# Optimization experiments

Hardware: AMD Instinct MI355X
Metric: run time of the kernel (lower is better)

## Reference

```python
import jax, jax.numpy as jnp
import numpy as np
import math

DIM = 1024
HEADS = 16
HEAD_DIM = DIM // HEADS
SCALE = math.sqrt(HEAD_DIM)


def setup_inputs() -> dict:
    key = jax.random.key(0)
    ks = jax.random.split(key, 7)
    B, T, C = 2, 2048, DIM
    w = 0.02
    return {
        "x": jax.random.normal(ks[0], (B, T, C), dtype=jnp.float32),
        "W_Q": jax.random.normal(ks[1], (C, C), dtype=jnp.float32) * w,
        "W_K": jax.random.normal(ks[2], (C, C), dtype=jnp.float32) * w,
        "W_V": jax.random.normal(ks[3], (C, C), dtype=jnp.float32) * w,
        "W_K_prime": jax.random.normal(ks[4], (C, C), dtype=jnp.float32) * w,
        "W_O": jax.random.normal(ks[5], (C, C), dtype=jnp.float32) * w,
        "alpha": jnp.float32(0.5),
    }


def _heads(y, B, T):
    # (B,T,C) -> (B,H,T,D)
    return y.reshape(B, T, HEADS, HEAD_DIM).transpose(0, 2, 1, 3)


def reference(x, W_Q, W_K, W_V, W_K_prime, W_O, alpha):
    B, T, C = x.shape
    # nn.Linear(no bias): y = x @ W.T
    q = _heads(x @ W_Q.T, B, T)
    k = _heads(x @ W_K.T, B, T)
    v = _heads(x @ W_V.T, B, T)
    kp = _heads(x @ W_K_prime.T, B, T)

    # Standard branch
    scores = jnp.einsum("bhqd,bhkd->bhqk", q, k) / SCALE
    attn = jax.nn.softmax(scores, axis=-1)  # dropout = identity (eval mode)
    out_std = jnp.einsum("bhqk,bhkd->bhqd", attn, v)

    # K' branch
    scores_p = jnp.einsum("bhqd,bhkd->bhqk", q, kp) / SCALE
    attn_p = jax.nn.softmax(scores_p, axis=-1)
    out_p = jnp.einsum("bhqk,bhkd->bhqd", attn_p, v)

    out = alpha * out_std + (1.0 - alpha) * out_p
    out = out.transpose(0, 2, 1, 3).reshape(B, T, C)
    return out @ W_O.T
```

## Files before the change

kernel.cpp:

```cpp
#include <hip/hip_runtime.h>
#include <math.h>

#define TSZ 2048
#define CDIM 1024

typedef __attribute__((ext_vector_type(8))) short s16x8;
typedef __attribute__((ext_vector_type(4))) float f32x4;
typedef __attribute__((ext_vector_type(16))) float f32x16;
typedef __attribute__((ext_vector_type(2))) unsigned int u32x2;
typedef __attribute__((ext_vector_type(4))) unsigned int u32x4;

#define QSCL 0.1803368801f

__device__ __forceinline__ short f2bf(float f) {
    union { float f; unsigned u; } v; v.f = f;
    unsigned r = v.u + 0x7fffu + ((v.u >> 16) & 1u);
    return (short)(r >> 16);
}
__device__ __forceinline__ unsigned cvtpk(float lo, float hi) {
    unsigned r;
    asm("v_cvt_pk_bf16_f32 %0, %1, %2" : "=v"(r) : "v"(lo), "v"(hi));
    return r;
}
__device__ __forceinline__ float fexp2(float x) {
    float r;
    asm("v_exp_f32 %0, %1" : "=v"(r) : "v"(x));
    return r;
}
__device__ __forceinline__ s16x8 u2s(u32x4 u) {
    union { u32x4 u; s16x8 s; } c; c.u = u; return c.s;
}
__device__ __forceinline__ f32x16 mfma32(s16x8 a, s16x8 b, f32x16 c) {
    return __builtin_amdgcn_mfma_f32_32x32x16_bf16(a, b, c, 0, 0, 0);
}

__global__ void cast_f32_bf16(const float* __restrict__ src, short* __restrict__ dst, int n4) {
    int i = blockIdx.x * blockDim.x + threadIdx.x;
    int stride = gridDim.x * blockDim.x;
    for (; i < n4; i += stride) {
        float4 v = reinterpret_cast<const float4*>(src)[i];
        short4 o;
        o.x = f2bf(v.x); o.y = f2bf(v.y); o.z = f2bf(v.z); o.w = f2bf(v.w);
        reinterpret_cast<short4*>(dst)[i] = o;
    }
}

__global__ void cast_w5(const float* __restrict__ w0, const float* __restrict__ w1,
                        const float* __restrict__ w2, const float* __restrict__ w3,
                        const float* __restrict__ w4,
                        short* __restrict__ o0, short* __restrict__ o1,
                        short* __restrict__ o2, short* __restrict__ o3,
                        short* __restrict__ o4) {
    int z = blockIdx.y;
    const float* s = z == 0 ? w0 : z == 1 ? w1 : z == 2 ? w2 : z == 3 ? w3 : w4;
    short* d = z == 0 ? o0 : z == 1 ? o1 : z == 2 ? o2 : z == 3 ? o3 : o4;
    int i = blockIdx.x * blockDim.x + threadIdx.x;
    float4 v = reinterpret_cast<const float4*>(s)[i];
    short4 o;
    o.x = f2bf(v.x); o.y = f2bf(v.y); o.z = f2bf(v.z); o.w = f2bf(v.w);
    reinterpret_cast<short4*>(d)[i] = o;
}

__device__ __forceinline__ void gload16(const short* g, short* l) {
    __builtin_amdgcn_global_load_lds((const __attribute__((address_space(1))) void*)g,
                                     (__attribute__((address_space(3))) void*)l, 16, 0, 0);
}

__device__ __forceinline__ void stage128x64(short* lds_t, const short* g, int ld, int tid, int w) {
    #pragma unroll
    for (int call = 0; call < 4; ++call) {
        int c = call * 256 + tid;
        int row = c >> 3;
        int sc = (c & 7) ^ (row & 7);
        gload16(g + (size_t)row * ld + sc * 8, lds_t + (size_t)(call * 256 + w * 64) * 8);
    }
}

__device__ __forceinline__ void stage64x64(short* lds_t, const short* g, int ld, int tid, int w) {
    #pragma unroll
    for (int call = 0; call < 2; ++call) {
        int c = call * 256 + tid;
        int row = c >> 3;
        int sc = (c & 7) ^ (row & 7);
        gload16(g + (size_t)row * ld + sc * 8, lds_t + (size_t)(call * 256 + w * 64) * 8);
    }
}

__device__ __forceinline__ s16x8 frag_read(const short* tile, int row, int kc) {
    const char* p = (const char*)tile + row * 128 + (((kc ^ (row & 7)) & 7) << 4);
    return *reinterpret_cast<const s16x8*>(p);
}

__global__ __launch_bounds__(256) void gemm4_proj(
    const short* __restrict__ xb,
    const short* __restrict__ w0, const short* __restrict__ w1,
    const short* __restrict__ w2, const short* __restrict__ w3,
    short* __restrict__ o0, short* __restrict__ o1,
    short* __restrict__ o2, short* __restrict__ o3)
{
    __shared__ short sA[128 * 64], sB[128 * 64];
    int tid = threadIdx.x, lane = tid & 63, w = tid >> 6;
    int wrow = w >> 1, wcol = w & 1;
    int z = blockIdx.y;
    const short* W = z == 0 ? w0 : z == 1 ? w1 : z == 2 ? w2 : w3;
    short* outp = z == 0 ? o0 : z == 1 ? o1 : z == 2 ? o2 : o3;
    int bx = blockIdx.x;
    bx = (bx & 7) * 32 + (bx >> 3);
    int r0 = (bx >> 3) * 128;
    int c0 = (bx & 7) * 128;

    f32x4 zero = {0.f, 0.f, 0.f, 0.f};
    f32x4 acc[4][4];
    #pragma unroll
    for (int i = 0; i < 4; ++i)
        #pragma unroll
        for (int j = 0; j < 4; ++j) acc[i][j] = zero;

    for (int kt = 0; kt < 16; ++kt) {
        __syncthreads();
        stage128x64(sA, xb + (size_t)r0 * CDIM + kt * 64, CDIM, tid, w);
        stage128x64(sB, W + (size_t)c0 * CDIM + kt * 64, CDIM, tid, w);
        __syncthreads();
        #pragma unroll
        for (int ks = 0; ks < 2; ++ks) {
            int kc = ks * 4 + (lane >> 4);
            s16x8 af[4], bfr[4];
            #pragma unroll
            for (int mt = 0; mt < 4; ++mt) af[mt] = frag_read(sA, wrow * 64 + mt * 16 + (lane & 15), kc);
            #pragma unroll
            for (int nt = 0; nt < 4; ++nt) bfr[nt] = frag_read(sB, wcol * 64 + nt * 16 + (lane & 15), kc);
            #pragma unroll
            for (int mt = 0; mt < 4; ++mt)
                #pragma unroll
                for (int nt = 0; nt < 4; ++nt)
                    acc[mt][nt] = __builtin_amdgcn_mfma_f32_16x16x32_bf16(af[mt], bfr[nt], acc[mt][nt], 0, 0, 0);
        }
    }

    bool vt_mode = (z == 2);
    float oscale = (z == 0) ? QSCL : 1.0f;
    #pragma unroll
    for (int mt = 0; mt < 4; ++mt)
        #pragma unroll
        for (int nt = 0; nt < 4; ++nt)
            #pragma unroll
            for (int jr = 0; jr < 4; ++jr) {
                int gi = r0 + wrow * 64 + mt * 16 + ((lane >> 4) << 2) + jr;
                int gn = c0 + wcol * 64 + nt * 16 + (lane & 15);
                short v = f2bf(acc[mt][nt][jr] * oscale);
                int b = gi >> 11, t = gi & 2047, h = gn >> 6, d = gn & 63;
                size_t off;
                if (!vt_mode) off = ((size_t)(b * 16 + h) * TSZ + t) * 64 + d;
                else          off = ((size_t)(b * 16 + h) * 64 + d) * TSZ + t;
                outp[off] = v;
            }
}

__global__ __launch_bounds__(256) void gemm_final(
    const short* __restrict__ ab, const short* __restrict__ wo, float* __restrict__ out)
{
    __shared__ short sA[128 * 64], sB[128 * 64];
    int tid = threadIdx.x, lane = tid & 63, w = tid >> 6;
    int wrow = w >> 1, wcol = w & 1;
    int bx = blockIdx.x;
    bx = (bx & 7) * 32 + (bx >> 3);
    int r0 = (bx >> 3) * 128;
    int c0 = (bx & 7) * 128;

    f32x4 zero = {0.f, 0.f, 0.f, 0.f};
    f32x4 acc[4][4];
    #pragma unroll
    for (int i = 0; i < 4; ++i)
        #pragma unroll
        for (int j = 0; j < 4; ++j) acc[i][j] = zero;

    for (int kt = 0; kt < 16; ++kt) {
        __syncthreads();
        stage128x64(sA, ab + (size_t)r0 * CDIM + kt * 64, CDIM, tid, w);
        stage128x64(sB, wo + (size_t)c0 * CDIM + kt * 64, CDIM, tid, w);
        __syncthreads();
        #pragma unroll
        for (int ks = 0; ks < 2; ++ks) {
            int kc = ks * 4 + (lane >> 4);
            s16x8 af[4], bfr[4];
            #pragma unroll
            for (int mt = 0; mt < 4; ++mt) af[mt] = frag_read(sA, wrow * 64 + mt * 16 + (lane & 15), kc);
            #pragma unroll
            for (int nt = 0; nt < 4; ++nt) bfr[nt] = frag_read(sB, wcol * 64 + nt * 16 + (lane & 15), kc);
            #pragma unroll
            for (int mt = 0; mt < 4; ++mt)
                #pragma unroll
                for (int nt = 0; nt < 4; ++nt)
                    acc[mt][nt] = __builtin_amdgcn_mfma_f32_16x16x32_bf16(af[mt], bfr[nt], acc[mt][nt], 0, 0, 0);
        }
    }

    #pragma unroll
    for (int mt = 0; mt < 4; ++mt)
        #pragma unroll
        for (int nt = 0; nt < 4; ++nt)
            #pragma unroll
            for (int jr = 0; jr < 4; ++jr) {
                int gi = r0 + wrow * 64 + mt * 16 + ((lane >> 4) << 2) + jr;
                int gn = c0 + wcol * 64 + nt * 16 + (lane & 15);
                out[(size_t)gi * CDIM + gn] = acc[mt][nt][jr];
            }
}

__global__ __launch_bounds__(256, 2) void attn_fused(
    const short* __restrict__ q, const short* __restrict__ k, const short* __restrict__ kp,
    const short* __restrict__ vt, const float* __restrict__ alphap, short* __restrict__ aout)
{
    __shared__ short sK[2][64 * 64], sKp[2][64 * 64], sV[2][64 * 64];
    int tid = threadIdx.x, lane = tid & 63, w = tid >> 6;
    int h = lane >> 5, l31 = lane & 31;

    int id = blockIdx.x + gridDim.x * blockIdx.y;
    int nid = (id & 7) * 64 + (id >> 3);
    int bh = nid >> 4;
    int qt0 = (nid & 15) * 128;

    const short* Q  = q  + (size_t)bh * TSZ * 64;
    const short* K  = k  + (size_t)bh * TSZ * 64;
    const short* Kp = kp + (size_t)bh * TSZ * 64;
    const short* Vt = vt + (size_t)bh * 64 * TSZ;

    int qrow = qt0 + w * 32 + l31;
    s16x8 qf[4];
    #pragma unroll
    for (int s = 0; s < 4; ++s)
        qf[s] = *reinterpret_cast<const s16x8*>(Q + (size_t)qrow * 64 + s * 16 + h * 8);

    f32x16 o[2][2];
    #pragma unroll
    for (int br = 0; br < 2; ++br)
        #pragma unroll
        for (int dt = 0; dt < 2; ++dt)
            #pragma unroll
            for (int r = 0; r < 16; ++r) o[br][dt][r] = 0.f;
    float lloc[2] = {0.f, 0.f};

    stage64x64(sK[0],  K, 64, tid, w);
    stage64x64(sKp[0], Kp, 64, tid, w);
    stage64x64(sV[0],  Vt, TSZ, tid, w);
    __syncthreads();

    int cur = 0;
    for (int kt = 0; kt < 32; ++kt) {
        if (kt < 31) {
            int t0n = (kt + 1) * 64;
            stage64x64(sK[cur ^ 1],  K  + (size_t)t0n * 64, 64, tid, w);
            stage64x64(sKp[cur ^ 1], Kp + (size_t)t0n * 64, 64, tid, w);
            stage64x64(sV[cur ^ 1],  Vt + t0n, TSZ, tid, w);
        }
        const short* kbuf0 = sK[cur];
        const short* kbuf1 = sKp[cur];
        const short* vbuf  = sV[cur];

        u32x4 pfrag[2][4];
        #pragma unroll
        for (int br = 0; br < 2; ++br) {
            const short* kb = br == 0 ? kbuf0 : kbuf1;
            f32x16 sa0, sa1;
            #pragma unroll
            for (int r = 0; r < 16; ++r) { sa0[r] = 0.f; sa1[r] = 0.f; }
            __builtin_amdgcn_s_setprio(1);
            #pragma unroll
            for (int s = 0; s < 4; ++s) {
                s16x8 af0 = frag_read(kb, l31,      2 * s + h);
                s16x8 af1 = frag_read(kb, 32 + l31, 2 * s + h);
                sa0 = mfma32(af0, qf[s], sa0);
                sa1 = mfma32(af1, qf[s], sa1);
            }
            __builtin_amdgcn_s_setprio(0);

            float p0 = 0.f, p1 = 0.f, p2 = 0.f, p3 = 0.f;
            #pragma unroll
            for (int r = 0; r < 16; r += 4) {
                sa0[r]     = fexp2(sa0[r]);     p0 += sa0[r];
                sa0[r + 1] = fexp2(sa0[r + 1]); p1 += sa0[r + 1];
                sa0[r + 2] = fexp2(sa0[r + 2]); p2 += sa0[r + 2];
                sa0[r + 3] = fexp2(sa0[r + 3]); p3 += sa0[r + 3];
                sa1[r]     = fexp2(sa1[r]);     p0 += sa1[r];
                sa1[r + 1] = fexp2(sa1[r + 1]); p1 += sa1[r + 1];
                sa1[r + 2] = fexp2(sa1[r + 2]); p2 += sa1[r + 2];
                sa1[r + 3] = fexp2(sa1[r + 3]); p3 += sa1[r + 3];
            }
            lloc[br] += (p0 + p1) + (p2 + p3);

            #pragma unroll
            for (int t = 0; t < 2; ++t) {
                const f32x16* sap = t ? &sa1 : &sa0;
                unsigned pk[8];
                #pragma unroll
                for (int i = 0; i < 8; ++i)
                    pk[i] = cvtpk((*sap)[2 * i], (*sap)[2 * i + 1]);
                u32x2 r02 = __builtin_amdgcn_permlane32_swap(pk[0], pk[2], false, false);
                u32x2 r13 = __builtin_amdgcn_permlane32_swap(pk[1], pk[3], false, false);
                u32x2 r46 = __builtin_amdgcn_permlane32_swap(pk[4], pk[6], false, false);
                u32x2 r57 = __builtin_amdgcn_permlane32_swap(pk[5], pk[7], false, false);
                u32x4 fA, fB;
                fA[0] = r02[0]; fA[1] = r13[0]; fA[2] = r02[1]; fA[3] = r13[1];
                fB[0] = r46[0]; fB[1] = r57[0]; fB[2] = r46[1]; fB[3] = r57[1];
                pfrag[br][2 * t] = fA;
                pfrag[br][2 * t + 1] = fB;
            }
        }

        __builtin_amdgcn_s_setprio(1);
        #pragma unroll
        for (int s = 0; s < 4; ++s)
            #pragma unroll
            for (int dt = 0; dt < 2; ++dt) {
                s16x8 vf = frag_read(vbuf, dt * 32 + l31, 2 * s + h);
                o[0][dt] = mfma32(vf, u2s(pfrag[0][s]), o[0][dt]);
                o[1][dt] = mfma32(vf, u2s(pfrag[1][s]), o[1][dt]);
            }
        __builtin_amdgcn_s_setprio(0);

        __syncthreads();
        cur ^= 1;
    }

    float lsum0 = lloc[0] + __shfl_xor(lloc[0], 32, 64);
    float lsum1 = lloc[1] + __shfl_xor(lloc[1], 32, 64);
    float alpha = alphap[0];
    float a0 = alpha / lsum0;
    float a1 = (1.f - alpha) / lsum1;
    int b = bh >> 4, hh = bh & 15;
    int t = qt0 + w * 32 + l31;
    size_t rowbase = ((size_t)(b * TSZ + t)) * CDIM + hh * 64;
    #pragma unroll
    for (int dt = 0; dt < 2; ++dt)
        #pragma unroll
        for (int g = 0; g < 4; ++g) {
            short4 v4;
            #pragma unroll
            for (int j = 0; j < 4; ++j) {
                int r = 4 * g + j;
                float v = a0 * o[0][dt][r] + a1 * o[1][dt][r];
                ((short*)&v4)[j] = f2bf(v);
            }
            *reinterpret_cast<short4*>(aout + rowbase + dt * 32 + g * 8 + h * 4) = v4;
        }
}

extern "C" void kernel_launch(void* const* d_in, const int* in_sizes, int n_in,
                              void* d_out, int out_size, void* d_ws, size_t ws_size,
                              hipStream_t stream)
{
    const float* x     = (const float*)d_in[0];
    const float* WQ    = (const float*)d_in[1];
    const float* WK    = (const float*)d_in[2];
    const float* WV    = (const float*)d_in[3];
    const float* WKp   = (const float*)d_in[4];
    const float* WO    = (const float*)d_in[5];
    const float* alpha = (const float*)d_in[6];
    float* out = (float*)d_out;

    char* ws = (char*)d_ws;
    const size_t MB = 1024 * 1024;
    short* xb   = (short*)(ws + 0);
    short* wqb  = (short*)(ws + 8 * MB);
    short* wkb  = (short*)(ws + 10 * MB);
    short* wvb  = (short*)(ws + 12 * MB);
    short* wkpb = (short*)(ws + 14 * MB);
    short* wob  = (short*)(ws + 16 * MB);
    short* qb   = (short*)(ws + 18 * MB);
    short* kb   = (short*)(ws + 26 * MB);
    short* kpb  = (short*)(ws + 34 * MB);
    short* vtb  = (short*)(ws + 42 * MB);
    short* anb  = (short*)(ws + 50 * MB);

    cast_f32_bf16<<<2048, 256, 0, stream>>>(x, xb, (TSZ * 2 * CDIM) / 4);
    cast_w5<<<dim3(1024, 5), 256, 0, stream>>>(WQ, WK, WV, WKp, WO,
                                               wqb, wkb, wvb, wkpb, wob);

    gemm4_proj<<<dim3(256, 4), 256, 0, stream>>>(xb, wqb, wkb, wvb, wkpb, qb, kb, vtb, kpb);
    attn_fused<<<dim3(16, 32), 256, 0, stream>>>(qb, kb, kpb, vtb, alpha, anb);
    gemm_final<<<dim3(256), 256, 0, stream>>>(anb, wob, out);
}
```

Measured before the change: 161.3 us.

## Split attention waves by branch and merge weight and input cast kernels

The attention kernel now gives each wave a single branch (K or K') over 64 queries instead of both branches over 32 queries. Each K fragment read from LDS then feeds two query blocks, which halves LDS fragment traffic per MFMA. The two branch results are combined through a swizzled fp32 LDS exchange and an extra barrier at the end. The x cast and the weight casts are also merged into one launch to save a kernel launch. The cost is more live registers (two Q fragment sets and four score accumulators), which could strain the 2-block-per-CU launch bound, plus the epilogue exchange.

```diff
diff --git a/kernel.cpp b/kernel.cpp
--- a/kernel.cpp
+++ b/kernel.cpp
@@ -34,31 +34,31 @@
     return __builtin_amdgcn_mfma_f32_32x32x16_bf16(a, b, c, 0, 0, 0);
 }
 
-__global__ void cast_f32_bf16(const float* __restrict__ src, short* __restrict__ dst, int n4) {
+__global__ void cast_all(const float* __restrict__ x,
+                         const float* __restrict__ w0, const float* __restrict__ w1,
+                         const float* __restrict__ w2, const float* __restrict__ w3,
+                         const float* __restrict__ w4,
+                         short* __restrict__ xb,
+                         short* __restrict__ o0, short* __restrict__ o1,
+                         short* __restrict__ o2, short* __restrict__ o3,
+                         short* __restrict__ o4) {
+    int z = blockIdx.y;
     int i = blockIdx.x * blockDim.x + threadIdx.x;
-    int stride = gridDim.x * blockDim.x;
-    for (; i < n4; i += stride) {
-        float4 v = reinterpret_cast<const float4*>(src)[i];
+    if (z == 0) {
+        for (int j = i; j < (TSZ * 2 * CDIM) / 4; j += 1024 * 256) {
+            float4 v = reinterpret_cast<const float4*>(x)[j];
+            short4 o;
+            o.x = f2bf(v.x); o.y = f2bf(v.y); o.z = f2bf(v.z); o.w = f2bf(v.w);
+            reinterpret_cast<short4*>(xb)[j] = o;
+        }
+    } else {
+        const float* s = z == 1 ? w0 : z == 2 ? w1 : z == 3 ? w2 : z == 4 ? w3 : w4;
+        short* d = z == 1 ? o0 : z == 2 ? o1 : z == 3 ? o2 : z == 4 ? o3 : o4;
+        float4 v = reinterpret_cast<const float4*>(s)[i];
         short4 o;
         o.x = f2bf(v.x); o.y = f2bf(v.y); o.z = f2bf(v.z); o.w = f2bf(v.w);
-        reinterpret_cast<short4*>(dst)[i] = o;
-    }
-}
-
-__global__ void cast_w5(const float* __restrict__ w0, const float* __restrict__ w1,
-                        const float* __restrict__ w2, const float* __restrict__ w3,
-                        const float* __restrict__ w4,
-                        short* __restrict__ o0, short* __restrict__ o1,
-                        short* __restrict__ o2, short* __restrict__ o3,
-                        short* __restrict__ o4) {
-    int z = blockIdx.y;
-    const float* s = z == 0 ? w0 : z == 1 ? w1 : z == 2 ? w2 : z == 3 ? w3 : w4;
-    short* d = z == 0 ? o0 : z == 1 ? o1 : z == 2 ? o2 : z == 3 ? o3 : o4;
-    int i = blockIdx.x * blockDim.x + threadIdx.x;
-    float4 v = reinterpret_cast<const float4*>(s)[i];
-    short4 o;
-    o.x = f2bf(v.x); o.y = f2bf(v.y); o.z = f2bf(v.z); o.w = f2bf(v.w);
-    reinterpret_cast<short4*>(d)[i] = o;
+        reinterpret_cast<short4*>(d)[i] = o;
+    }
 }
 
 __device__ __forceinline__ void gload16(const short* g, short* l) {
@@ -211,90 +211,96 @@
     const short* __restrict__ q, const short* __restrict__ k, const short* __restrict__ kp,
     const short* __restrict__ vt, const float* __restrict__ alphap, short* __restrict__ aout)
 {
-    __shared__ short sK[2][64 * 64], sKp[2][64 * 64], sV[2][64 * 64];
+    __shared__ short sbuf[6][64 * 64];
     int tid = threadIdx.x, lane = tid & 63, w = tid >> 6;
     int h = lane >> 5, l31 = lane & 31;
+    int qg = w >> 1, br = w & 1;
 
     int id = blockIdx.x + gridDim.x * blockIdx.y;
     int nid = (id & 7) * 64 + (id >> 3);
     int bh = nid >> 4;
     int qt0 = (nid & 15) * 128;
 
-    const short* Q  = q  + (size_t)bh * TSZ * 64;
-    const short* K  = k  + (size_t)bh * TSZ * 64;
-    const short* Kp = kp + (size_t)bh * TSZ * 64;
-    const short* Vt = vt + (size_t)bh * 64 * TSZ;
-
-    int qrow = qt0 + w * 32 + l31;
-    s16x8 qf[4];
-    #pragma unroll
-    for (int s = 0; s < 4; ++s)
-        qf[s] = *reinterpret_cast<const s16x8*>(Q + (size_t)qrow * 64 + s * 16 + h * 8);
+    const short* Q   = q  + (size_t)bh * TSZ * 64;
+    const short* Kg  = k  + (size_t)bh * TSZ * 64;
+    const short* Kpg = kp + (size_t)bh * TSZ * 64;
+    const short* Vt  = vt + (size_t)bh * 64 * TSZ;
+
+    s16x8 qf[2][4];
+    #pragma unroll
+    for (int qb = 0; qb < 2; ++qb)
+        #pragma unroll
+        for (int s = 0; s < 4; ++s)
+            qf[qb][s] = *reinterpret_cast<const s16x8*>(
+                Q + (size_t)(qt0 + qg * 64 + qb * 32 + l31) * 64 + s * 16 + h * 8);
 
     f32x16 o[2][2];
     #pragma unroll
-    for (int br = 0; br < 2; ++br)
+    for (int qb = 0; qb < 2; ++qb)
         #pragma unroll
         for (int dt = 0; dt < 2; ++dt)
             #pragma unroll
-            for (int r = 0; r < 16; ++r) o[br][dt][r] = 0.f;
+            for (int r = 0; r < 16; ++r) o[qb][dt][r] = 0.f;
     float lloc[2] = {0.f, 0.f};
 
-    stage64x64(sK[0],  K, 64, tid, w);
-    stage64x64(sKp[0], Kp, 64, tid, w);
-    stage64x64(sV[0],  Vt, TSZ, tid, w);
+    stage64x64(sbuf[0], Kg, 64, tid, w);
+    stage64x64(sbuf[2], Kpg, 64, tid, w);
+    stage64x64(sbuf[4], Vt, TSZ, tid, w);
     __syncthreads();
 
     int cur = 0;
     for (int kt = 0; kt < 32; ++kt) {
         if (kt < 31) {
             int t0n = (kt + 1) * 64;
-            stage64x64(sK[cur ^ 1],  K  + (size_t)t0n * 64, 64, tid, w);
-            stage64x64(sKp[cur ^ 1], Kp + (size_t)t0n * 64, 64, tid, w);
-            stage64x64(sV[cur ^ 1],  Vt + t0n, TSZ, tid, w);
-        }
-        const short* kbuf0 = sK[cur];
-        const short* kbuf1 = sKp[cur];
-        const short* vbuf  = sV[cur];
+            stage64x64(sbuf[cur ^ 1],       Kg  + (size_t)t0n * 64, 64, tid, w);
+            stage64x64(sbuf[2 + (cur ^ 1)], Kpg + (size_t)t0n * 64, 64, tid, w);
+            stage64x64(sbuf[4 + (cur ^ 1)], Vt + t0n, TSZ, tid, w);
+        }
+        const short* kbuf = br ? sbuf[2 + cur] : sbuf[cur];
+        const short* vbuf = sbuf[4 + cur];
+
+        f32x16 sa[2][2];
+        #pragma unroll
+        for (int qb = 0; qb < 2; ++qb)
+            #pragma unroll
+            for (int hf = 0; hf < 2; ++hf)
+                #pragma unroll
+                for (int r = 0; r < 16; ++r) sa[qb][hf][r] = 0.f;
+        __builtin_amdgcn_s_setprio(1);
+        #pragma unroll
+        for (int s = 0; s < 4; ++s) {
+            s16x8 af0 = frag_read(kbuf, l31,      2 * s + h);
+            s16x8 af1 = frag_read(kbuf, 32 + l31, 2 * s + h);
+            sa[0][0] = mfma32(af0, qf[0][s], sa[0][0]);
+            sa[0][1] = mfma32(af1, qf[0][s], sa[0][1]);
+            sa[1][0] = mfma32(af0, qf[1][s], sa[1][0]);
+            sa[1][1] = mfma32(af1, qf[1][s], sa[1][1]);
+        }
+        __builtin_amdgcn_s_setprio(0);
 
         u32x4 pfrag[2][4];
         #pragma unroll
-        for (int br = 0; br < 2; ++br) {
-            const short* kb = br == 0 ? kbuf0 : kbuf1;
-            f32x16 sa0, sa1;
-            #pragma unroll
-            for (int r = 0; r < 16; ++r) { sa0[r] = 0.f; sa1[r] = 0.f; }
-            __builtin_amdgcn_s_setprio(1);
-            #pragma unroll
-            for (int s = 0; s < 4; ++s) {
-                s16x8 af0 = frag_read(kb, l31,      2 * s + h);
-                s16x8 af1 = frag_read(kb, 32 + l31, 2 * s + h);
-                sa0 = mfma32(af0, qf[s], sa0);
-                sa1 = mfma32(af1, qf[s], sa1);
+        for (int qb = 0; qb < 2; ++qb) {
+            float p0 = 0.f, p1 = 0.f, p2 = 0.f, p3 = 0.f;
+            #pragma unroll
+            for (int r = 0; r < 16; r += 4) {
+                sa[qb][0][r]     = fexp2(sa[qb][0][r]);     p0 += sa[qb][0][r];
+                sa[qb][0][r + 1] = fexp2(sa[qb][0][r + 1]); p1 += sa[qb][0][r + 1];
+                sa[qb][0][r + 2] = fexp2(sa[qb][0][r + 2]); p2 += sa[qb][0][r + 2];
+                sa[qb][0][r + 3] = fexp2(sa[qb][0][r + 3]); p3 += sa[qb][0][r + 3];
+                sa[qb][1][r]     = fexp2(sa[qb][1][r]);     p0 += sa[qb][1][r];
+                sa[qb][1][r + 1] = fexp2(sa[qb][1][r + 1]); p1 += sa[qb][1][r + 1];
+                sa[qb][1][r + 2] = fexp2(sa[qb][1][r + 2]); p2 += sa[qb][1][r + 2];
+                sa[qb][1][r + 3] = fexp2(sa[qb][1][r + 3]); p3 += sa[qb][1][r + 3];
             }
-            __builtin_amdgcn_s_setprio(0);
-
-            float p0 = 0.f, p1 = 0.f, p2 = 0.f, p3 = 0.f;
-            #pragma unroll
-            for (int r = 0; r < 16; r += 4) {
-                sa0[r]     = fexp2(sa0[r]);     p0 += sa0[r];
-                sa0[r + 1] = fexp2(sa0[r + 1]); p1 += sa0[r + 1];
-                sa0[r + 2] = fexp2(sa0[r + 2]); p2 += sa0[r + 2];
-                sa0[r + 3] = fexp2(sa0[r + 3]); p3 += sa0[r + 3];
-                sa1[r]     = fexp2(sa1[r]);     p0 += sa1[r];
-                sa1[r + 1] = fexp2(sa1[r + 1]); p1 += sa1[r + 1];
-                sa1[r + 2] = fexp2(sa1[r + 2]); p2 += sa1[r + 2];
-                sa1[r + 3] = fexp2(sa1[r + 3]); p3 += sa1[r + 3];
-            }
-            lloc[br] += (p0 + p1) + (p2 + p3);
+            lloc[qb] += (p0 + p1) + (p2 + p3);
 
             #pragma unroll
             for (int t = 0; t < 2; ++t) {
-                const f32x16* sap = t ? &sa1 : &sa0;
                 unsigned pk[8];
                 #pragma unroll
                 for (int i = 0; i < 8; ++i)
-                    pk[i] = cvtpk((*sap)[2 * i], (*sap)[2 * i + 1]);
+                    pk[i] = cvtpk(sa[qb][t][2 * i], sa[qb][t][2 * i + 1]);
                 u32x2 r02 = __builtin_amdgcn_permlane32_swap(pk[0], pk[2], false, false);
                 u32x2 r13 = __builtin_amdgcn_permlane32_swap(pk[1], pk[3], false, false);
                 u32x2 r46 = __builtin_amdgcn_permlane32_swap(pk[4], pk[6], false, false);
@@ -302,8 +308,8 @@
                 u32x4 fA, fB;
                 fA[0] = r02[0]; fA[1] = r13[0]; fA[2] = r02[1]; fA[3] = r13[1];
                 fB[0] = r46[0]; fB[1] = r57[0]; fB[2] = r46[1]; fB[3] = r57[1];
-                pfrag[br][2 * t] = fA;
-                pfrag[br][2 * t + 1] = fB;
+                pfrag[qb][2 * t] = fA;
+                pfrag[qb][2 * t + 1] = fB;
             }
         }
 
@@ -322,27 +328,56 @@
         cur ^= 1;
     }
 
-    float lsum0 = lloc[0] + __shfl_xor(lloc[0], 32, 64);
-    float lsum1 = lloc[1] + __shfl_xor(lloc[1], 32, 64);
     float alpha = alphap[0];
-    float a0 = alpha / lsum0;
-    float a1 = (1.f - alpha) / lsum1;
-    int b = bh >> 4, hh = bh & 15;
-    int t = qt0 + w * 32 + l31;
-    size_t rowbase = ((size_t)(b * TSZ + t)) * CDIM + hh * 64;
-    #pragma unroll
-    for (int dt = 0; dt < 2; ++dt)
-        #pragma unroll
-        for (int g = 0; g < 4; ++g) {
-            short4 v4;
-            #pragma unroll
-            for (int j = 0; j < 4; ++j) {
-                int r = 4 * g + j;
-                float v = a0 * o[0][dt][r] + a1 * o[1][dt][r];
-                ((short*)&v4)[j] = f2bf(v);
-            }
-            *reinterpret_cast<short4*>(aout + rowbase + dt * 32 + g * 8 + h * 4) = v4;
-        }
+    float cb = br ? (1.f - alpha) : alpha;
+    float inv[2];
+    #pragma unroll
+    for (int qb = 0; qb < 2; ++qb) {
+        float ls = lloc[qb] + __shfl_xor(lloc[qb], 32, 64);
+        inv[qb] = cb / ls;
+    }
+
+    float* sX = (float*)&sbuf[0][0];
+    if (br) {
+        #pragma unroll
+        for (int qb = 0; qb < 2; ++qb)
+            #pragma unroll
+            for (int dt = 0; dt < 2; ++dt)
+                #pragma unroll
+                for (int g = 0; g < 4; ++g) {
+                    int qloc = qg * 64 + qb * 32 + l31;
+                    int dsw = (dt * 32 + g * 8 + h * 4) ^ ((l31 & 7) << 3);
+                    float4 v4;
+                    v4.x = o[qb][dt][4 * g + 0] * inv[qb];
+                    v4.y = o[qb][dt][4 * g + 1] * inv[qb];
+                    v4.z = o[qb][dt][4 * g + 2] * inv[qb];
+                    v4.w = o[qb][dt][4 * g + 3] * inv[qb];
+                    *reinterpret_cast<float4*>(sX + qloc * 64 + dsw) = v4;
+                }
+    }
+    __syncthreads();
+    if (!br) {
+        int b = bh >> 4, hh = bh & 15;
+        #pragma unroll
+        for (int qb = 0; qb < 2; ++qb) {
+            int t = qt0 + qg * 64 + qb * 32 + l31;
+            size_t rowbase = ((size_t)(b * TSZ + t)) * CDIM + hh * 64;
+            #pragma unroll
+            for (int dt = 0; dt < 2; ++dt)
+                #pragma unroll
+                for (int g = 0; g < 4; ++g) {
+                    int qloc = qg * 64 + qb * 32 + l31;
+                    int dsw = (dt * 32 + g * 8 + h * 4) ^ ((l31 & 7) << 3);
+                    float4 p = *reinterpret_cast<const float4*>(sX + qloc * 64 + dsw);
+                    short4 v4;
+                    v4.x = f2bf(o[qb][dt][4 * g + 0] * inv[qb] + p.x);
+                    v4.y = f2bf(o[qb][dt][4 * g + 1] * inv[qb] + p.y);
+                    v4.z = f2bf(o[qb][dt][4 * g + 2] * inv[qb] + p.z);
+                    v4.w = f2bf(o[qb][dt][4 * g + 3] * inv[qb] + p.w);
+                    *reinterpret_cast<short4*>(aout + rowbase + dt * 32 + g * 8 + h * 4) = v4;
+                }
+        }
+    }
 }
 
 extern "C" void kernel_launch(void* const* d_in, const int* in_sizes, int n_in,
@@ -372,9 +407,8 @@
     short* vtb  = (short*)(ws + 42 * MB);
     short* anb  = (short*)(ws + 50 * MB);
 
-    cast_f32_bf16<<<2048, 256, 0, stream>>>(x, xb, (TSZ * 2 * CDIM) / 4);
-    cast_w5<<<dim3(1024, 5), 256, 0, stream>>>(WQ, WK, WV, WKp, WO,
-                                               wqb, wkb, wvb, wkpb, wob);
+    cast_all<<<dim3(1024, 6), 256, 0, stream>>>(x, WQ, WK, WV, WKp, WO,
+                                                xb, wqb, wkb, wvb, wkpb, wob);
 
     gemm4_proj<<<dim3(256, 4), 256, 0, stream>>>(xb, wqb, wkb, wvb, wkpb, qb, kb, vtb, kpb);
     attn_fused<<<dim3(16, 32), 256, 0, stream>>>(qb, kb, kpb, vtb, alpha, anb);
```

Result: faster. 156.6 us, median of 2 (-2.9%).
